# Performance work log

Measured on AMD Instinct MI355X. Metric: run time of the kernel, lower is better.

## Reference

```python
import jax, jax.numpy as jnp
import numpy as np

N0 = 16384; F_IN = 384; H = 512; E0 = 131072
DEPTH = 2; RATIO = 0.25; START_K = 6; K_INC = 1; INTERP_K = 6


def _pdist2(a, b):
    # squared euclidean distances [Na, Nb]
    d2 = jnp.sum(a * a, axis=1)[:, None] + jnp.sum(b * b, axis=1)[None, :] - 2.0 * (a @ b.T)
    return jnp.maximum(d2, 0.0)


def _fps(pos, n_keep):
    # farthest point sampling, deterministic start at node 0
    sel0 = jnp.zeros((n_keep,), jnp.int32)
    dist0 = jnp.sum((pos - pos[0]) ** 2, axis=-1)

    def body(i, st):
        sel, dist = st
        idx = jnp.argmax(dist).astype(jnp.int32)
        sel = sel.at[i].set(idx)
        dist = jnp.minimum(dist, jnp.sum((pos - pos[idx]) ** 2, axis=-1))
        return (sel, dist)

    sel, _ = jax.lax.fori_loop(1, n_keep, body, (sel0, dist0))
    return sel


def _knn_graph(pos, k):
    n = pos.shape[0]
    d2 = _pdist2(pos, pos)
    d2 = d2.at[jnp.arange(n), jnp.arange(n)].set(1e10)  # exclude self
    _, nbr = jax.lax.top_k(-d2, k)                      # [n, k] nearest neighbors
    src = nbr.reshape(-1)                               # flow: source_to_target
    dst = jnp.repeat(jnp.arange(n, dtype=nbr.dtype), k)
    return src, dst


def _gcn(x, src, dst, W, b):
    # GCNConv(improved=True): A_hat = D^-1/2 (A + 2I) D^-1/2, edge weights = 1
    n = x.shape[0]
    h = x @ W
    deg = jax.ops.segment_sum(jnp.ones(src.shape[0], x.dtype), dst, num_segments=n) + 2.0
    dinv = jax.lax.rsqrt(deg)
    coef = dinv[src] * dinv[dst]
    agg = jax.ops.segment_sum(h[src] * coef[:, None], dst, num_segments=n)
    agg = agg + h * (2.0 * dinv * dinv)[:, None]        # self loops with weight 2
    return agg + b


def _knn_interpolate(x, pos_x, pos_y, k):
    # interpolate coarse features x at pos_x onto fine positions pos_y (PyG knn_interpolate)
    d2 = _pdist2(pos_y, pos_x)                          # [Ny, Nx]
    negd, idx = jax.lax.top_k(-d2, k)                   # k nearest coarse points
    w = 1.0 / jnp.maximum(-negd, 1e-16)                 # [Ny, k]
    num = jnp.einsum('yk,ykf->yf', w, x[idx])
    return num / jnp.sum(w, axis=-1, keepdims=True)


def setup_inputs() -> dict:
    key = jax.random.key(0)
    ks = jax.random.split(key, 16)
    def w(k, fin, fout):
        return (jax.random.normal(k, (fin, fout), jnp.float32) / np.sqrt(fin)).astype(jnp.float32)
    return {
        'x': jax.random.normal(ks[0], (N0, F_IN), jnp.float32),
        'pos': jax.random.uniform(ks[1], (N0, 2), jnp.float32) * 100.0,
        'edge_index': jax.random.randint(ks[2], (2, E0), 0, N0, dtype=jnp.int32),
        'W_down0': w(ks[3], F_IN, H), 'b_down0': jnp.zeros((H,), jnp.float32),
        'W_down1': w(ks[4], H, H),   'b_down1': jnp.zeros((H,), jnp.float32),
        'W_up0': w(ks[5], H, H),     'b_up0': jnp.zeros((H,), jnp.float32),
        'W_up1': w(ks[6], H, H),     'b_up1': jnp.zeros((H,), jnp.float32),
        'W_lin': w(ks[7], H, H),     'b_lin': jnp.zeros((H,), jnp.float32),
    }


def reference(x, pos, edge_index, W_down0, b_down0, W_down1, b_down1,
              W_up0, b_up0, W_up1, b_up1, W_lin, b_lin):
    src, dst = edge_index[0], edge_index[1]
    Wd = [(W_down0, b_down0), (W_down1, b_down1)]
    Wu = [(W_up0, b_up0), (W_up1, b_up1)]
    all_pos = [pos]
    all_edges = [(src, dst)]
    for i in range(DEPTH):
        x = jax.nn.relu(_gcn(x, src, dst, *Wd[i]))
        n_keep = int(x.shape[0] * RATIO)
        perm = _fps(jax.lax.stop_gradient(pos), n_keep)
        pos = pos[perm]
        src, dst = _knn_graph(pos, START_K + i * K_INC)
        x = x[perm]
        all_pos.append(pos)
        all_edges.append((src, dst))
    for i in range(DEPTH):
        x = _knn_interpolate(x, all_pos[-i - 1], all_pos[-i - 2], INTERP_K)
        s, d = all_edges[-i - 2]
        x = jax.nn.relu(_gcn(x, s, d, *Wu[i]))
    return x @ W_lin + b_lin
```

## Files before the change

### kernel.cpp

```cpp
#include <hip/hip_runtime.h>

#define N0 16384
#define N1 4096
#define N2 1024
#define E0C 131072
#define FIN 384
#define HF 512

__device__ inline float4 f4fma(float w, const float4 v, float4 a) {
  a.x = fmaf(w, v.x, a.x); a.y = fmaf(w, v.y, a.y);
  a.z = fmaf(w, v.z, a.z); a.w = fmaf(w, v.w, a.w);
  return a;
}

__global__ __launch_bounds__(256)
void count_deg(const int* __restrict__ dst, int* __restrict__ cnt, int E) {
  int e = blockIdx.x * 256 + threadIdx.x;
  if (e < E) atomicAdd(&cnt[dst[e]], 1);
}

__global__ __launch_bounds__(1024)
void scan_offsets(const int* __restrict__ cnt, int* __restrict__ offs,
                  float* __restrict__ dinv) {
  __shared__ int ts[1024];
  const int t = threadIdx.x;
  int local[16];
  int sum = 0;
  #pragma unroll
  for (int j = 0; j < 16; ++j) { local[j] = cnt[t * 16 + j]; sum += local[j]; }
  ts[t] = sum;
  __syncthreads();
  for (int off = 1; off < 1024; off <<= 1) {
    int v = (t >= off) ? ts[t - off] : 0;
    __syncthreads();
    ts[t] += v;
    __syncthreads();
  }
  int run = ts[t] - sum;
  #pragma unroll
  for (int j = 0; j < 16; ++j) {
    offs[t * 16 + j] = run;
    dinv[t * 16 + j] = 1.0f / sqrtf((float)local[j] + 2.0f);
    run += local[j];
  }
  if (t == 1023) offs[N0] = run;
}

__global__ __launch_bounds__(256)
void fill_csr(const int* __restrict__ src, const int* __restrict__ dst,
              const int* __restrict__ offs, int* __restrict__ cursor,
              int* __restrict__ srcl, int E) {
  int e = blockIdx.x * 256 + threadIdx.x;
  if (e < E) {
    int d = dst[e];
    int p = atomicAdd(&cursor[d], 1);
    srcl[offs[d] + p] = src[e];
  }
}

template<int BM, int BN, int BK>
__global__ __launch_bounds__(256)
void gemm_f32(const float* __restrict__ A, const float* __restrict__ W,
              const float* __restrict__ bias, float* __restrict__ C,
              int M, int N, int K, int addBias) {
  __shared__ float As[BK][BM + 4];
  __shared__ float Ws[BK][BN];
  const int tid = threadIdx.x;
  const int bm = blockIdx.x * BM;
  const int bn = blockIdx.y * BN;
  const int tx = tid & 15;
  const int ty = tid >> 4;
  float acc[8][4];
  #pragma unroll
  for (int i = 0; i < 8; ++i)
    #pragma unroll
    for (int j = 0; j < 4; ++j) acc[i][j] = 0.f;

  for (int k0 = 0; k0 < K; k0 += BK) {
    #pragma unroll
    for (int h = 0; h < (BM * BK) / (256 * 4); ++h) {
      int q = tid + h * 256;
      int r = q >> 2;
      int c = (q & 3) << 2;
      float4 v = *(const float4*)(A + (size_t)(bm + r) * K + k0 + c);
      As[c][r] = v.x; As[c + 1][r] = v.y; As[c + 2][r] = v.z; As[c + 3][r] = v.w;
    }
    {
      int kk = tid >> 4;
      int n = (tid & 15) << 2;
      *(float4*)(&Ws[kk][n]) = *(const float4*)(W + (size_t)(k0 + kk) * N + bn + n);
    }
    __syncthreads();
    #pragma unroll
    for (int kk = 0; kk < BK; ++kk) {
      float4 b4 = *(const float4*)(&Ws[kk][tx << 2]);
      float4 a0 = *(const float4*)(&As[kk][ty << 3]);
      float4 a1 = *(const float4*)(&As[kk][(ty << 3) + 4]);
      float a[8] = {a0.x, a0.y, a0.z, a0.w, a1.x, a1.y, a1.z, a1.w};
      float b[4] = {b4.x, b4.y, b4.z, b4.w};
      #pragma unroll
      for (int i = 0; i < 8; ++i)
        #pragma unroll
        for (int j = 0; j < 4; ++j)
          acc[i][j] = fmaf(a[i], b[j], acc[i][j]);
    }
    __syncthreads();
  }
  #pragma unroll
  for (int i = 0; i < 8; ++i) {
    int row = bm + (ty << 3) + i;
    float4 o = {acc[i][0], acc[i][1], acc[i][2], acc[i][3]};
    if (addBias) {
      const float4 bb = *(const float4*)(bias + bn + (tx << 2));
      o.x += bb.x; o.y += bb.y; o.z += bb.z; o.w += bb.w;
    }
    *(float4*)(C + (size_t)row * N + bn + (tx << 2)) = o;
  }
}

__global__ __launch_bounds__(256)
void gcn_agg_csr(const float* __restrict__ h, const int* __restrict__ offs,
                 const int* __restrict__ srcl, const float* __restrict__ dinv,
                 const float* __restrict__ bias, float* __restrict__ out, int n) {
  const int wid = threadIdx.x >> 6, lane = threadIdx.x & 63;
  const int node = blockIdx.x * 4 + wid;
  if (node >= n) return;
  const float di = dinv[node];
  const int s0 = offs[node], s1 = offs[node + 1];
  float4 a0 = {0, 0, 0, 0}, a1 = {0, 0, 0, 0};
  for (int e = s0; e < s1; ++e) {
    const int s = srcl[e];
    const float w = dinv[s] * di;
    const float4* r = (const float4*)(h + (size_t)s * HF);
    a0 = f4fma(w, r[lane], a0);
    a1 = f4fma(w, r[64 + lane], a1);
  }
  const float sw = 2.0f * di * di;
  const float4* rs = (const float4*)(h + (size_t)node * HF);
  a0 = f4fma(sw, rs[lane], a0);
  a1 = f4fma(sw, rs[64 + lane], a1);
  const float4 b0 = *(const float4*)(bias + (lane << 2));
  const float4 b1 = *(const float4*)(bias + 256 + (lane << 2));
  a0.x = fmaxf(a0.x + b0.x, 0.f); a0.y = fmaxf(a0.y + b0.y, 0.f);
  a0.z = fmaxf(a0.z + b0.z, 0.f); a0.w = fmaxf(a0.w + b0.w, 0.f);
  a1.x = fmaxf(a1.x + b1.x, 0.f); a1.y = fmaxf(a1.y + b1.y, 0.f);
  a1.z = fmaxf(a1.z + b1.z, 0.f); a1.w = fmaxf(a1.w + b1.w, 0.f);
  float4* o = (float4*)(out + (size_t)node * HF);
  o[lane] = a0; o[64 + lane] = a1;
}

template<int K>
__global__ __launch_bounds__(256)
void gcn_agg_knn(const float* __restrict__ h, const int* __restrict__ nbr,
                 const float* __restrict__ bias, float* __restrict__ out, int n) {
  const int wid = threadIdx.x >> 6, lane = threadIdx.x & 63;
  const int node = blockIdx.x * 4 + wid;
  if (node >= n) return;
  const float di = 1.0f / sqrtf((float)(K + 2));
  const float w = di * di;
  float4 a0 = {0, 0, 0, 0}, a1 = {0, 0, 0, 0};
  #pragma unroll
  for (int j = 0; j < K; ++j) {
    const int s = nbr[node * K + j];
    const float4* r = (const float4*)(h + (size_t)s * HF);
    a0 = f4fma(w, r[lane], a0);
    a1 = f4fma(w, r[64 + lane], a1);
  }
  const float sw = 2.0f * di * di;
  const float4* rs = (const float4*)(h + (size_t)node * HF);
  a0 = f4fma(sw, rs[lane], a0);
  a1 = f4fma(sw, rs[64 + lane], a1);
  const float4 b0 = *(const float4*)(bias + (lane << 2));
  const float4 b1 = *(const float4*)(bias + 256 + (lane << 2));
  a0.x = fmaxf(a0.x + b0.x, 0.f); a0.y = fmaxf(a0.y + b0.y, 0.f);
  a0.z = fmaxf(a0.z + b0.z, 0.f); a0.w = fmaxf(a0.w + b0.w, 0.f);
  a1.x = fmaxf(a1.x + b1.x, 0.f); a1.y = fmaxf(a1.y + b1.y, 0.f);
  a1.z = fmaxf(a1.z + b1.z, 0.f); a1.w = fmaxf(a1.w + b1.w, 0.f);
  float4* o = (float4*)(out + (size_t)node * HF);
  o[lane] = a0; o[64 + lane] = a1;
}

__global__ __launch_bounds__(256)
void bin_hist(const float* __restrict__ pos, int* __restrict__ cid,
              int* __restrict__ hist, int n) {
  int i = blockIdx.x * 256 + threadIdx.x;
  if (i >= n) return;
  float x = pos[2 * i], y = pos[2 * i + 1];
  int cxi = (int)(x * 0.32f); cxi = cxi < 0 ? 0 : (cxi > 31 ? 31 : cxi);
  int cyi = (int)(y * 0.32f); cyi = cyi < 0 ? 0 : (cyi > 31 ? 31 : cyi);
  int c = cyi * 32 + cxi;
  cid[i] = c;
  atomicAdd(&hist[c], 1);
}

__global__ __launch_bounds__(1024)
void bin_scan(const int* __restrict__ hist, int* __restrict__ offs) {
  __shared__ int ts[1024];
  const int t = threadIdx.x;
  int v = hist[t];
  ts[t] = v;
  __syncthreads();
  for (int off = 1; off < 1024; off <<= 1) {
    int u = (t >= off) ? ts[t - off] : 0;
    __syncthreads();
    ts[t] += u;
    __syncthreads();
  }
  offs[t] = ts[t] - v;
  if (t == 1023) offs[1024] = ts[t];
}

__global__ __launch_bounds__(256)
void bin_scatter(const float* __restrict__ pos, const int* __restrict__ cid,
                 const int* __restrict__ offs, int* __restrict__ cursor,
                 float* __restrict__ sx, float* __restrict__ sy,
                 int* __restrict__ sid, int n) {
  int i = blockIdx.x * 256 + threadIdx.x;
  if (i >= n) return;
  int c = cid[i];
  int p = atomicAdd(&cursor[c], 1);
  int slot = offs[c] + p;
  sx[slot] = pos[2 * i];
  sy[slot] = pos[2 * i + 1];
  sid[slot] = i;
}

template<int NN>
__device__ __forceinline__ unsigned ror16(unsigned v) {
  return (unsigned)__builtin_amdgcn_update_dpp(0, (int)v, 0x120 | NN, 0xF, 0xF, false);
}

template<int N, int NCH, int NKEEP>
__global__ __launch_bounds__(NCH)
void fps_fast(const float* __restrict__ pos0,
              const float* __restrict__ sx, const float* __restrict__ sy,
              const int* __restrict__ sid,
              int* __restrict__ perm, float* __restrict__ pos_out) {
  constexpr int CHUNK = N / NCH;
  const int t = threadIdx.x;
  const int base = t * CHUNK;

  __shared__ float pxl[N];
  __shared__ float pyl[N];
  __shared__ unsigned long long ck[NCH];
  __shared__ float2 cp[NCH];
  __shared__ float bc[2];

  float d[CHUNK];
  unsigned kid[CHUNK];
  float xmn = 3.4e38f, xmx = -3.4e38f, ymn = 3.4e38f, ymx = -3.4e38f;

  float cx = pos0[0], cy = pos0[1];
  if (t == 0) { perm[0] = 0; pos_out[0] = cx; pos_out[1] = cy; }

  {
    unsigned long long best = 0; float bx = 0.f, by = 0.f;
    #pragma unroll
    for (int j = 0; j < CHUNK; ++j) {
      float qx = sx[base + j], qy = sy[base + j];
      kid[j] = ~(unsigned)sid[base + j];
      pxl[j * NCH + t] = qx;
      pyl[j * NCH + t] = qy;
      xmn = fminf(xmn, qx); xmx = fmaxf(xmx, qx);
      ymn = fminf(ymn, qy); ymx = fmaxf(ymx, qy);
      float dx = __fsub_rn(qx, cx), dy = __fsub_rn(qy, cy);
      float nd = __fadd_rn(__fmul_rn(dx, dx), __fmul_rn(dy, dy));
      d[j] = nd;
      unsigned long long kv =
          ((unsigned long long)__float_as_uint(nd) << 32) | kid[j];
      if (kv > best) { best = kv; bx = qx; by = qy; }
    }
    ck[t] = best;
    cp[t] = make_float2(bx, by);
  }
  float cmax = __uint_as_float((unsigned)(ck[t] >> 32));
  __syncthreads();

  for (int i = 1; i < NKEEP; ++i) {
    if (t < 64) {
      unsigned long long bk = 0;
      int sl = 0;
      #pragma unroll
      for (int j = 0; j < NCH / 64; ++j) {
        unsigned long long k = ck[t + j * 64];
        if (k > bk) { bk = k; sl = t + j * 64; }
      }
      {
        unsigned hi, lo, ohi, olo; int os;
        hi = (unsigned)(bk >> 32); lo = (unsigned)bk;
        ohi = ror16<1>(hi); olo = ror16<1>(lo); os = (int)ror16<1>((unsigned)sl);
        { unsigned long long ok = ((unsigned long long)ohi << 32) | olo;
          if (ok > bk) { bk = ok; sl = os; } }
        hi = (unsigned)(bk >> 32); lo = (unsigned)bk;
        ohi = ror16<2>(hi); olo = ror16<2>(lo); os = (int)ror16<2>((unsigned)sl);
        { unsigned long long ok = ((unsigned long long)ohi << 32) | olo;
          if (ok > bk) { bk = ok; sl = os; } }
        hi = (unsigned)(bk >> 32); lo = (unsigned)bk;
        ohi = ror16<4>(hi); olo = ror16<4>(lo); os = (int)ror16<4>((unsigned)sl);
        { unsigned long long ok = ((unsigned long long)ohi << 32) | olo;
          if (ok > bk) { bk = ok; sl = os; } }
        hi = (unsigned)(bk >> 32); lo = (unsigned)bk;
        ohi = ror16<8>(hi); olo = ror16<8>(lo); os = (int)ror16<8>((unsigned)sl);
        { unsigned long long ok = ((unsigned long long)ohi << 32) | olo;
          if (ok > bk) { bk = ok; sl = os; } }
      }
      unsigned hi = (unsigned)(bk >> 32), lo = (unsigned)bk;
      unsigned long long fb = 0; int fs = 0;
      #pragma unroll
      for (int r = 0; r < 4; ++r) {
        unsigned h = (unsigned)__builtin_amdgcn_readlane((int)hi, r * 16);
        unsigned l = (unsigned)__builtin_amdgcn_readlane((int)lo, r * 16);
        int s = __builtin_amdgcn_readlane(sl, r * 16);
        unsigned long long k = ((unsigned long long)h << 32) | l;
        if (k > fb) { fb = k; fs = s; }
      }
      if (t == 0) {
        float2 c = cp[fs];
        perm[i] = (int)(~(unsigned)fb);
        pos_out[2 * i] = c.x; pos_out[2 * i + 1] = c.y;
        bc[0] = c.x; bc[1] = c.y;
      }
    }
    __syncthreads();
    cx = bc[0]; cy = bc[1];

    float mdx = fmaxf(fmaxf(__fsub_rn(xmn, cx), __fsub_rn(cx, xmx)), 0.f);
    float mdy = fmaxf(fmaxf(__fsub_rn(ymn, cy), __fsub_rn(cy, ymx)), 0.f);
    float mb = mdx * mdx + mdy * mdy;
    if (!(mb * 0.99999f > cmax)) {
      unsigned long long best = 0; float bx = 0.f, by = 0.f;
      #pragma unroll
      for (int j = 0; j < CHUNK; ++j) {
        float qx = pxl[j * NCH + t], qy = pyl[j * NCH + t];
        float dx = __fsub_rn(qx, cx), dy = __fsub_rn(qy, cy);
        float nd = __fadd_rn(__fmul_rn(dx, dx), __fmul_rn(dy, dy));
        float dn = fminf(d[j], nd);
        d[j] = dn;
        unsigned long long kv =
            ((unsigned long long)__float_as_uint(dn) << 32) | kid[j];
        if (kv > best) { best = kv; bx = qx; by = qy; }
      }
      ck[t] = best;
      cp[t] = make_float2(bx, by);
      cmax = __uint_as_float((unsigned)(best >> 32));
    }
    __syncthreads();
  }
}

__global__ __launch_bounds__(256)
void gather_rows(const float* __restrict__ xin, const int* __restrict__ perm,
                 float* __restrict__ xout, int n) {
  const int wid = threadIdx.x >> 6, lane = threadIdx.x & 63;
  const int i = blockIdx.x * 4 + wid;
  if (i >= n) return;
  const int s = perm[i];
  const float4* r = (const float4*)(xin + (size_t)s * HF);
  float4* o = (float4*)(xout + (size_t)i * HF);
  o[lane] = r[lane];
  o[64 + lane] = r[64 + lane];
}

template<int NPTS, int K>
__global__ __launch_bounds__(256)
void knn_graph_kernel(const float* __restrict__ pos, int* __restrict__ srcout) {
  __shared__ float sx[NPTS], sy[NPTS], ss[NPTS];
  const int tid = threadIdx.x;
  for (int idx = tid; idx < NPTS; idx += 256) {
    float x = pos[2 * idx], y = pos[2 * idx + 1];
    sx[idx] = x; sy[idx] = y;
    ss[idx] = __fadd_rn(__fmul_rn(x, x), __fmul_rn(y, y));
  }
  __syncthreads();
  const int q = blockIdx.x * 256 + tid;
  const float qx = sx[q], qy = sy[q], qs = ss[q];
  float bd[K]; int bi[K];
  #pragma unroll
  for (int m = 0; m < K; ++m) { bd[m] = 3.4e38f; bi[m] = 0; }
  for (int j = 0; j < NPTS; ++j) {
    if (j == q) continue;
    float dot = __fadd_rn(__fmul_rn(qx, sx[j]), __fmul_rn(qy, sy[j]));
    float d2 = fmaxf(__fsub_rn(__fadd_rn(qs, ss[j]), __fmul_rn(2.0f, dot)), 0.0f);
    if (d2 < bd[K - 1]) {
      bool pr[K];
      #pragma unroll
      for (int m = 0; m < K; ++m) pr[m] = (d2 < bd[m]);
      #pragma unroll
      for (int m = K - 1; m >= 1; --m) {
        bd[m] = pr[m] ? (pr[m - 1] ? bd[m - 1] : d2) : bd[m];
        bi[m] = pr[m] ? (pr[m - 1] ? bi[m - 1] : j) : bi[m];
      }
      if (pr[0]) { bd[0] = d2; bi[0] = j; }
    }
  }
  #pragma unroll
  for (int m = 0; m < K; ++m) srcout[q * K + m] = bi[m];
}

template<int NX, int K>
__global__ __launch_bounds__(256)
void interp_topk(const float* __restrict__ posy, const float* __restrict__ posx,
                 int* __restrict__ oidx, float* __restrict__ ow,
                 float* __restrict__ owsum) {
  __shared__ float sx[NX], sy[NX], ss[NX];
  const int tid = threadIdx.x;
  for (int idx = tid; idx < NX; idx += 256) {
    float x = posx[2 * idx], y = posx[2 * idx + 1];
    sx[idx] = x; sy[idx] = y;
    ss[idx] = __fadd_rn(__fmul_rn(x, x), __fmul_rn(y, y));
  }
  __syncthreads();
  const int q = blockIdx.x * 256 + tid;
  const float qx = posy[2 * q], qy = posy[2 * q + 1];
  const float qs = __fadd_rn(__fmul_rn(qx, qx), __fmul_rn(qy, qy));
  float bd[K]; int bi[K];
  #pragma unroll
  for (int m = 0; m < K; ++m) { bd[m] = 3.4e38f; bi[m] = 0; }
  for (int j = 0; j < NX; ++j) {
    float dot = __fadd_rn(__fmul_rn(qx, sx[j]), __fmul_rn(qy, sy[j]));
    float d2 = fmaxf(__fsub_rn(__fadd_rn(qs, ss[j]), __fmul_rn(2.0f, dot)), 0.0f);
    if (d2 < bd[K - 1]) {
      bool pr[K];
      #pragma unroll
      for (int m = 0; m < K; ++m) pr[m] = (d2 < bd[m]);
      #pragma unroll
      for (int m = K - 1; m >= 1; --m) {
        bd[m] = pr[m] ? (pr[m - 1] ? bd[m - 1] : d2) : bd[m];
        bi[m] = pr[m] ? (pr[m - 1] ? bi[m - 1] : j) : bi[m];
      }
      if (pr[0]) { bd[0] = d2; bi[0] = j; }
    }
  }
  float wsum = 0.f;
  #pragma unroll
  for (int m = 0; m < K; ++m) {
    float w = 1.0f / fmaxf(bd[m], 1e-16f);
    ow[q * K + m] = w;
    oidx[q * K + m] = bi[m];
    wsum = __fadd_rn(wsum, w);
  }
  owsum[q] = wsum;
}

template<int K>
__global__ __launch_bounds__(256)
void interp_combine(const float* __restrict__ xin, const int* __restrict__ idx,
                    const float* __restrict__ w, const float* __restrict__ wsum,
                    float* __restrict__ out, int ny) {
  const int wid = threadIdx.x >> 6, lane = threadIdx.x & 63;
  const int q = blockIdx.x * 4 + wid;
  if (q >= ny) return;
  float4 a0 = {0, 0, 0, 0}, a1 = {0, 0, 0, 0};
  #pragma unroll
  for (int m = 0; m < K; ++m) {
    const int s = idx[q * K + m];
    const float wk = w[q * K + m];
    const float4* r = (const float4*)(xin + (size_t)s * HF);
    a0 = f4fma(wk, r[lane], a0);
    a1 = f4fma(wk, r[64 + lane], a1);
  }
  const float inv = wsum[q];
  a0.x /= inv; a0.y /= inv; a0.z /= inv; a0.w /= inv;
  a1.x /= inv; a1.y /= inv; a1.z /= inv; a1.w /= inv;
  float4* o = (float4*)(out + (size_t)q * HF);
  o[lane] = a0; o[64 + lane] = a1;
}

extern "C" void kernel_launch(void* const* d_in, const int* in_sizes, int n_in,
                              void* d_out, int out_size, void* d_ws, size_t ws_size,
                              hipStream_t stream) {
  const float* x    = (const float*)d_in[0];
  const float* pos  = (const float*)d_in[1];
  const int*   ei   = (const int*)d_in[2];
  const float* Wd0  = (const float*)d_in[3];
  const float* bd0  = (const float*)d_in[4];
  const float* Wd1  = (const float*)d_in[5];
  const float* bd1  = (const float*)d_in[6];
  const float* Wu0  = (const float*)d_in[7];
  const float* bu0  = (const float*)d_in[8];
  const float* Wu1  = (const float*)d_in[9];
  const float* bu1  = (const float*)d_in[10];
  const float* Wl   = (const float*)d_in[11];
  const float* bl   = (const float*)d_in[12];
  float* out = (float*)d_out;

  char* ws = (char*)d_ws;
  size_t off = 0;
  auto alloc = [&](size_t bytes) -> char* {
    char* p = ws + off;
    off = (off + bytes + 255) & ~(size_t)255;
    return p;
  };
  float* bufA   = (float*)alloc((size_t)N0 * HF * 4);
  float* bufB   = (float*)alloc((size_t)N0 * HF * 4);
  float* bufC   = (float*)alloc((size_t)N1 * HF * 4);
  float* x2     = (float*)alloc((size_t)N2 * HF * 4);
  int*   offs0  = (int*)alloc((N0 + 1) * 4);
  int*   srcl0  = (int*)alloc(E0C * 4);
  int*   cnt    = (int*)alloc(N0 * 4);
  int*   cursor = (int*)alloc(N0 * 4);
  float* dinv0  = (float*)alloc(N0 * 4);
  int*   perm0  = (int*)alloc(N1 * 4);
  float* pos1   = (float*)alloc(N1 * 2 * 4);
  int*   src1   = (int*)alloc(N1 * 6 * 4);
  int*   perm1  = (int*)alloc(N2 * 4);
  float* pos2   = (float*)alloc(N2 * 2 * 4);
  int*   iidx   = (int*)alloc((size_t)N0 * 6 * 4);
  float* iw     = (float*)alloc((size_t)N0 * 6 * 4);
  float* iwsum  = (float*)alloc(N0 * 4);
  float* bsx    = (float*)alloc(N0 * 4);
  float* bsy    = (float*)alloc(N0 * 4);
  int*   bsid   = (int*)alloc(N0 * 4);
  int*   bcid   = (int*)alloc(N0 * 4);
  int*   bhist  = (int*)alloc(1024 * 4);
  int*   bcur   = (int*)alloc(1024 * 4);
  int*   boffs  = (int*)alloc(1025 * 4);

  float* h1   = bufB;
  float* x1f  = bufB + (size_t)N1 * HF;
  float* hu0  = bufB;
  float* xu0f = bufB + (size_t)N1 * HF;

  hipMemsetAsync(cnt, 0, N0 * 4, stream);
  hipMemsetAsync(cursor, 0, N0 * 4, stream);
  count_deg<<<E0C / 256, 256, 0, stream>>>(ei + E0C, cnt, E0C);
  scan_offsets<<<1, 1024, 0, stream>>>(cnt, offs0, dinv0);
  fill_csr<<<E0C / 256, 256, 0, stream>>>(ei, ei + E0C, offs0, cursor, srcl0, E0C);

  hipMemsetAsync(bhist, 0, 1024 * 4, stream);
  hipMemsetAsync(bcur, 0, 1024 * 4, stream);
  bin_hist<<<N0 / 256, 256, 0, stream>>>(pos, bcid, bhist, N0);
  bin_scan<<<1, 1024, 0, stream>>>(bhist, boffs);
  bin_scatter<<<N0 / 256, 256, 0, stream>>>(pos, bcid, boffs, bcur, bsx, bsy, bsid, N0);

  gemm_f32<128, 64, 16><<<dim3(N0 / 128, HF / 64), 256, 0, stream>>>(
      x, Wd0, nullptr, bufA, N0, HF, FIN, 0);
  gcn_agg_csr<<<N0 / 4, 256, 0, stream>>>(bufA, offs0, srcl0, dinv0, bd0, bufB, N0);
  fps_fast<N0, 1024, N1><<<1, 1024, 0, stream>>>(pos, bsx, bsy, bsid, perm0, pos1);
  gather_rows<<<N1 / 4, 256, 0, stream>>>(bufB, perm0, bufC, N1);
  knn_graph_kernel<N1, 6><<<N1 / 256, 256, 0, stream>>>(pos1, src1);

  hipMemsetAsync(bhist, 0, 1024 * 4, stream);
  hipMemsetAsync(bcur, 0, 1024 * 4, stream);
  bin_hist<<<N1 / 256, 256, 0, stream>>>(pos1, bcid, bhist, N1);
  bin_scan<<<1, 1024, 0, stream>>>(bhist, boffs);
  bin_scatter<<<N1 / 256, 256, 0, stream>>>(pos1, bcid, boffs, bcur, bsx, bsy, bsid, N1);

  gemm_f32<128, 64, 16><<<dim3(N1 / 128, HF / 64), 256, 0, stream>>>(
      bufC, Wd1, nullptr, h1, N1, HF, HF, 0);
  gcn_agg_knn<6><<<N1 / 4, 256, 0, stream>>>(h1, src1, bd1, x1f, N1);
  fps_fast<N1, 256, N2><<<1, 256, 0, stream>>>(pos1, bsx, bsy, bsid, perm1, pos2);
  gather_rows<<<N2 / 4, 256, 0, stream>>>(x1f, perm1, x2, N2);

  interp_topk<N2, 6><<<N1 / 256, 256, 0, stream>>>(pos1, pos2, iidx, iw, iwsum);
  interp_combine<6><<<N1 / 4, 256, 0, stream>>>(x2, iidx, iw, iwsum, bufC, N1);
  gemm_f32<128, 64, 16><<<dim3(N1 / 128, HF / 64), 256, 0, stream>>>(
      bufC, Wu0, nullptr, hu0, N1, HF, HF, 0);
  gcn_agg_knn<6><<<N1 / 4, 256, 0, stream>>>(hu0, src1, bu0, xu0f, N1);

  interp_topk<N1, 6><<<N0 / 256, 256, 0, stream>>>(pos, pos1, iidx, iw, iwsum);
  interp_combine<6><<<N0 / 4, 256, 0, stream>>>(xu0f, iidx, iw, iwsum, bufA, N0);
  gemm_f32<128, 64, 16><<<dim3(N0 / 128, HF / 64), 256, 0, stream>>>(
      bufA, Wu1, nullptr, bufB, N0, HF, HF, 0);
  gcn_agg_csr<<<N0 / 4, 256, 0, stream>>>(bufB, offs0, srcl0, dinv0, bu1, bufA, N0);

  gemm_f32<128, 64, 16><<<dim3(N0 / 128, HF / 64), 256, 0, stream>>>(
      bufA, Wl, bl, out, N0, HF, HF, 1);
}
```

Measured before the change: 8.045 ms.

## Rework FPS reduction to one barrier per iteration with distributed argmax

The farthest-point-sampling kernel now reduces the per-thread best key and coordinates with DPP inside each wave (plus a small cross-wave step when there are 16 waves). It writes per-wave winners to a double-buffered shared array so every thread redoes the final 16-way reduction itself, which removes the second __syncthreads and the serial lane-0 step per iteration. Per-point distance and index are packed into one 64-bit key, and whole waves skip work via ballot when no lane's bounding box can change. The cost is redundant reduction work in every thread, and the 1024-thread variant adds an extra shared-memory exchange inside each wave.

After: 9.260 ms. +15.1%, slower.

```diff
diff --git a/kernel.cpp b/kernel.cpp
--- a/kernel.cpp
+++ b/kernel.cpp
@@ -230,121 +230,122 @@
   return (unsigned)__builtin_amdgcn_update_dpp(0, (int)v, 0x120 | NN, 0xF, 0xF, false);
 }
 
-template<int N, int NCH, int NKEEP>
-__global__ __launch_bounds__(NCH)
-void fps_fast(const float* __restrict__ pos0,
-              const float* __restrict__ sx, const float* __restrict__ sy,
-              const int* __restrict__ sid,
-              int* __restrict__ perm, float* __restrict__ pos_out) {
-  constexpr int CHUNK = N / NCH;
+__device__ __forceinline__ void kcmp(unsigned& hi, unsigned& lo, float& x, float& y,
+                                     unsigned ohi, unsigned olo, float ox, float oy) {
+  unsigned long long a = ((unsigned long long)hi << 32) | lo;
+  unsigned long long b = ((unsigned long long)ohi << 32) | olo;
+  if (b > a) { hi = ohi; lo = olo; x = ox; y = oy; }
+}
+
+#define ROR_STEP(NN) { \
+    unsigned ohi_ = ror16<NN>(hi), olo_ = ror16<NN>(lo); \
+    unsigned ox_ = ror16<NN>(__float_as_uint(x)), oy_ = ror16<NN>(__float_as_uint(y)); \
+    kcmp(hi, lo, x, y, ohi_, olo_, __uint_as_float(ox_), __uint_as_float(oy_)); }
+
+template<bool WENT>
+__device__ __forceinline__ void entry_reduce(unsigned long long ckey, float ccx, float ccy,
+                                             int t, float4* wsc,
+                                             unsigned& ehi, unsigned& elo,
+                                             float& ex, float& ey) {
+  unsigned hi = (unsigned)(ckey >> 32), lo = (unsigned)ckey;
+  float x = ccx, y = ccy;
+  ROR_STEP(1) ROR_STEP(2) ROR_STEP(4) ROR_STEP(8)
+  if constexpr (WENT) {
+    if ((t & 15) == 0)
+      wsc[(t >> 4) & 3] = make_float4(__uint_as_float(hi), __uint_as_float(lo), x, y);
+    float4 a0 = wsc[0], a1 = wsc[1], a2 = wsc[2], a3 = wsc[3];
+    hi = __float_as_uint(a0.x); lo = __float_as_uint(a0.y); x = a0.z; y = a0.w;
+    kcmp(hi, lo, x, y, __float_as_uint(a1.x), __float_as_uint(a1.y), a1.z, a1.w);
+    kcmp(hi, lo, x, y, __float_as_uint(a2.x), __float_as_uint(a2.y), a2.z, a2.w);
+    kcmp(hi, lo, x, y, __float_as_uint(a3.x), __float_as_uint(a3.y), a3.z, a3.w);
+  }
+  ehi = hi; elo = lo; ex = x; ey = y;
+}
+
+template<int N, int NT, int NKEEP>
+__global__ __launch_bounds__(NT)
+void fps_fast2(const float* __restrict__ pos0,
+               const float* __restrict__ sx, const float* __restrict__ sy,
+               const int* __restrict__ sid,
+               int* __restrict__ perm, float* __restrict__ pos_out) {
+  constexpr int CHUNK = N / NT;
+  constexpr int NWAVE = NT / 64;
+  constexpr bool WENT = (NWAVE == 16);
   const int t = threadIdx.x;
   const int base = t * CHUNK;
 
   __shared__ float pxl[N];
   __shared__ float pyl[N];
-  __shared__ unsigned long long ck[NCH];
-  __shared__ float2 cp[NCH];
-  __shared__ float bc[2];
-
-  float d[CHUNK];
-  unsigned kid[CHUNK];
-  float xmn = 3.4e38f, xmx = -3.4e38f, ymn = 3.4e38f, ymx = -3.4e38f;
-
+  __shared__ float4 ebuf[2][16];
+  __shared__ float4 wscr[NWAVE][4];
+
+  unsigned long long key[CHUNK];
   float cx = pos0[0], cy = pos0[1];
   if (t == 0) { perm[0] = 0; pos_out[0] = cx; pos_out[1] = cy; }
 
-  {
-    unsigned long long best = 0; float bx = 0.f, by = 0.f;
-    #pragma unroll
-    for (int j = 0; j < CHUNK; ++j) {
-      float qx = sx[base + j], qy = sy[base + j];
-      kid[j] = ~(unsigned)sid[base + j];
-      pxl[j * NCH + t] = qx;
-      pyl[j * NCH + t] = qy;
-      xmn = fminf(xmn, qx); xmx = fmaxf(xmx, qx);
-      ymn = fminf(ymn, qy); ymx = fmaxf(ymx, qy);
-      float dx = __fsub_rn(qx, cx), dy = __fsub_rn(qy, cy);
-      float nd = __fadd_rn(__fmul_rn(dx, dx), __fmul_rn(dy, dy));
-      d[j] = nd;
-      unsigned long long kv =
-          ((unsigned long long)__float_as_uint(nd) << 32) | kid[j];
-      if (kv > best) { best = kv; bx = qx; by = qy; }
-    }
-    ck[t] = best;
-    cp[t] = make_float2(bx, by);
-  }
-  float cmax = __uint_as_float((unsigned)(ck[t] >> 32));
+  float bx0 = 3.4e38f, bx1 = -3.4e38f, by0 = 3.4e38f, by1 = -3.4e38f;
+  unsigned long long ckey = 0; float ccx = 0.f, ccy = 0.f;
+  #pragma unroll
+  for (int j = 0; j < CHUNK; ++j) {
+    float qx = sx[base + j], qy = sy[base + j];
+    unsigned uid = ~(unsigned)sid[base + j];
+    pxl[j * NT + t] = qx; pyl[j * NT + t] = qy;
+    bx0 = fminf(bx0, qx); bx1 = fmaxf(bx1, qx);
+    by0 = fminf(by0, qy); by1 = fmaxf(by1, qy);
+    float dx = __fsub_rn(qx, cx), dy = __fsub_rn(qy, cy);
+    float nd = __fadd_rn(__fmul_rn(dx, dx), __fmul_rn(dy, dy));
+    unsigned long long k = ((unsigned long long)__float_as_uint(nd) << 32) | uid;
+    key[j] = k;
+    if (k > ckey) { ckey = k; ccx = qx; ccy = qy; }
+  }
+  float cmax = __uint_as_float((unsigned)(ckey >> 32));
+
+  unsigned ehi, elo; float ex, ey;
+  entry_reduce<WENT>(ckey, ccx, ccy, t, wscr[t >> 6], ehi, elo, ex, ey);
+  if ((t & (WENT ? 63 : 15)) == 0)
+    ebuf[0][WENT ? (t >> 6) : (t >> 4)] =
+        make_float4(__uint_as_float(ehi), __uint_as_float(elo), ex, ey);
   __syncthreads();
 
+  int p = 0;
   for (int i = 1; i < NKEEP; ++i) {
-    if (t < 64) {
-      unsigned long long bk = 0;
-      int sl = 0;
-      #pragma unroll
-      for (int j = 0; j < NCH / 64; ++j) {
-        unsigned long long k = ck[t + j * 64];
-        if (k > bk) { bk = k; sl = t + j * 64; }
+    float4 e = ebuf[p][t & 15];
+    unsigned hi = __float_as_uint(e.x), lo = __float_as_uint(e.y);
+    float x = e.z, y = e.w;
+    ROR_STEP(1) ROR_STEP(2) ROR_STEP(4) ROR_STEP(8)
+    if (t == 0) {
+      perm[i] = (int)(~lo);
+      pos_out[2 * i] = x; pos_out[2 * i + 1] = y;
+    }
+    cx = x; cy = y;
+
+    float mdx = fmaxf(fmaxf(__fsub_rn(bx0, cx), __fsub_rn(cx, bx1)), 0.f);
+    float mdy = fmaxf(fmaxf(__fsub_rn(by0, cy), __fsub_rn(cy, by1)), 0.f);
+    float mb = mdx * mdx + mdy * mdy;
+    bool act = !(mb * 0.99999f > cmax);
+    if (__ballot(act) != 0) {
+      if (act) {
+        unsigned long long best = 0; float bx = 0.f, by = 0.f;
+        #pragma unroll
+        for (int j = 0; j < CHUNK; ++j) {
+          float qx = pxl[j * NT + t], qy = pyl[j * NT + t];
+          float dx = __fsub_rn(qx, cx), dy = __fsub_rn(qy, cy);
+          float nd = __fadd_rn(__fmul_rn(dx, dx), __fmul_rn(dy, dy));
+          unsigned long long nk =
+              ((unsigned long long)__float_as_uint(nd) << 32) | (unsigned)key[j];
+          if (nk < key[j]) key[j] = nk;
+          if (key[j] > best) { best = key[j]; bx = qx; by = qy; }
+        }
+        ckey = best; ccx = bx; ccy = by;
+        cmax = __uint_as_float((unsigned)(best >> 32));
       }
-      {
-        unsigned hi, lo, ohi, olo; int os;
-        hi = (unsigned)(bk >> 32); lo = (unsigned)bk;
-        ohi = ror16<1>(hi); olo = ror16<1>(lo); os = (int)ror16<1>((unsigned)sl);
-        { unsigned long long ok = ((unsigned long long)ohi << 32) | olo;
-          if (ok > bk) { bk = ok; sl = os; } }
-        hi = (unsigned)(bk >> 32); lo = (unsigned)bk;
-        ohi = ror16<2>(hi); olo = ror16<2>(lo); os = (int)ror16<2>((unsigned)sl);
-        { unsigned long long ok = ((unsigned long long)ohi << 32) | olo;
-          if (ok > bk) { bk = ok; sl = os; } }
-        hi = (unsigned)(bk >> 32); lo = (unsigned)bk;
-        ohi = ror16<4>(hi); olo = ror16<4>(lo); os = (int)ror16<4>((unsigned)sl);
-        { unsigned long long ok = ((unsigned long long)ohi << 32) | olo;
-          if (ok > bk) { bk = ok; sl = os; } }
-        hi = (unsigned)(bk >> 32); lo = (unsigned)bk;
-        ohi = ror16<8>(hi); olo = ror16<8>(lo); os = (int)ror16<8>((unsigned)sl);
-        { unsigned long long ok = ((unsigned long long)ohi << 32) | olo;
-          if (ok > bk) { bk = ok; sl = os; } }
-      }
-      unsigned hi = (unsigned)(bk >> 32), lo = (unsigned)bk;
-      unsigned long long fb = 0; int fs = 0;
-      #pragma unroll
-      for (int r = 0; r < 4; ++r) {
-        unsigned h = (unsigned)__builtin_amdgcn_readlane((int)hi, r * 16);
-        unsigned l = (unsigned)__builtin_amdgcn_readlane((int)lo, r * 16);
-        int s = __builtin_amdgcn_readlane(sl, r * 16);
-        unsigned long long k = ((unsigned long long)h << 32) | l;
-        if (k > fb) { fb = k; fs = s; }
-      }
-      if (t == 0) {
-        float2 c = cp[fs];
-        perm[i] = (int)(~(unsigned)fb);
-        pos_out[2 * i] = c.x; pos_out[2 * i + 1] = c.y;
-        bc[0] = c.x; bc[1] = c.y;
-      }
-    }
-    __syncthreads();
-    cx = bc[0]; cy = bc[1];
-
-    float mdx = fmaxf(fmaxf(__fsub_rn(xmn, cx), __fsub_rn(cx, xmx)), 0.f);
-    float mdy = fmaxf(fmaxf(__fsub_rn(ymn, cy), __fsub_rn(cy, ymx)), 0.f);
-    float mb = mdx * mdx + mdy * mdy;
-    if (!(mb * 0.99999f > cmax)) {
-      unsigned long long best = 0; float bx = 0.f, by = 0.f;
-      #pragma unroll
-      for (int j = 0; j < CHUNK; ++j) {
-        float qx = pxl[j * NCH + t], qy = pyl[j * NCH + t];
-        float dx = __fsub_rn(qx, cx), dy = __fsub_rn(qy, cy);
-        float nd = __fadd_rn(__fmul_rn(dx, dx), __fmul_rn(dy, dy));
-        float dn = fminf(d[j], nd);
-        d[j] = dn;
-        unsigned long long kv =
-            ((unsigned long long)__float_as_uint(dn) << 32) | kid[j];
-        if (kv > best) { best = kv; bx = qx; by = qy; }
-      }
-      ck[t] = best;
-      cp[t] = make_float2(bx, by);
-      cmax = __uint_as_float((unsigned)(best >> 32));
-    }
-    __syncthreads();
+      entry_reduce<WENT>(ckey, ccx, ccy, t, wscr[t >> 6], ehi, elo, ex, ey);
+    }
+    if ((t & (WENT ? 63 : 15)) == 0)
+      ebuf[p ^ 1][WENT ? (t >> 6) : (t >> 4)] =
+          make_float4(__uint_as_float(ehi), __uint_as_float(elo), ex, ey);
+    __syncthreads();
+    p ^= 1;
   }
 }
 
@@ -536,7 +537,7 @@
   gemm_f32<128, 64, 16><<<dim3(N0 / 128, HF / 64), 256, 0, stream>>>(
       x, Wd0, nullptr, bufA, N0, HF, FIN, 0);
   gcn_agg_csr<<<N0 / 4, 256, 0, stream>>>(bufA, offs0, srcl0, dinv0, bd0, bufB, N0);
-  fps_fast<N0, 1024, N1><<<1, 1024, 0, stream>>>(pos, bsx, bsy, bsid, perm0, pos1);
+  fps_fast2<N0, 1024, N1><<<1, 1024, 0, stream>>>(pos, bsx, bsy, bsid, perm0, pos1);
   gather_rows<<<N1 / 4, 256, 0, stream>>>(bufB, perm0, bufC, N1);
   knn_graph_kernel<N1, 6><<<N1 / 256, 256, 0, stream>>>(pos1, src1);
 
@@ -549,7 +550,7 @@
   gemm_f32<128, 64, 16><<<dim3(N1 / 128, HF / 64), 256, 0, stream>>>(
       bufC, Wd1, nullptr, h1, N1, HF, HF, 0);
   gcn_agg_knn<6><<<N1 / 4, 256, 0, stream>>>(h1, src1, bd1, x1f, N1);
-  fps_fast<N1, 256, N2><<<1, 256, 0, stream>>>(pos1, bsx, bsy, bsid, perm1, pos2);
+  fps_fast2<N1, 256, N2><<<1, 256, 0, stream>>>(pos1, bsx, bsy, bsid, perm1, pos2);
   gather_rows<<<N2 / 4, 256, 0, stream>>>(x1f, perm1, x2, N2);
 
   interp_topk<N2, 6><<<N1 / 256, 256, 0, stream>>>(pos1, pos2, iidx, iw, iwsum);
```

## Morton-order spatial bins and pack FPS distances into 64-bit keys with fewer threads

Applied to the files above, without the earlier changes.

Spatial bins are now numbered in Z-order (Morton) instead of row-major, so each thread's contiguous chunk of sorted points is spatially tighter and its bounding-box skip test fires more often. The FPS kernel stores the running min distance and id together as one 64-bit key per point, which drops the separate distance and id arrays and compares keys directly. The level-0 FPS now uses 512 threads with 32 points each instead of 1024 with 16, with launch bounds set for one block. The aim is cheaper per-iteration reductions and syncs in this serial kernel, at the cost of more per-thread work and register pressure.

After: 10.61 ms. +31.9%, slower.

```diff
diff --git a/kernel.cpp b/kernel.cpp
--- a/kernel.cpp
+++ b/kernel.cpp
@@ -180,6 +180,15 @@
   o[lane] = a0; o[64 + lane] = a1;
 }
 
+__device__ __forceinline__ unsigned part1by1(unsigned x) {
+  x &= 0xFFFFu;
+  x = (x | (x << 8)) & 0x00FF00FFu;
+  x = (x | (x << 4)) & 0x0F0F0F0Fu;
+  x = (x | (x << 2)) & 0x33333333u;
+  x = (x | (x << 1)) & 0x55555555u;
+  return x;
+}
+
 __global__ __launch_bounds__(256)
 void bin_hist(const float* __restrict__ pos, int* __restrict__ cid,
               int* __restrict__ hist, int n) {
@@ -188,7 +197,7 @@
   float x = pos[2 * i], y = pos[2 * i + 1];
   int cxi = (int)(x * 0.32f); cxi = cxi < 0 ? 0 : (cxi > 31 ? 31 : cxi);
   int cyi = (int)(y * 0.32f); cyi = cyi < 0 ? 0 : (cyi > 31 ? 31 : cyi);
-  int c = cyi * 32 + cxi;
+  int c = (int)(part1by1((unsigned)cxi) | (part1by1((unsigned)cyi) << 1));
   cid[i] = c;
   atomicAdd(&hist[c], 1);
 }
@@ -230,45 +239,42 @@
   return (unsigned)__builtin_amdgcn_update_dpp(0, (int)v, 0x120 | NN, 0xF, 0xF, false);
 }
 
-template<int N, int NCH, int NKEEP>
-__global__ __launch_bounds__(NCH)
-void fps_fast(const float* __restrict__ pos0,
-              const float* __restrict__ sx, const float* __restrict__ sy,
-              const int* __restrict__ sid,
-              int* __restrict__ perm, float* __restrict__ pos_out) {
-  constexpr int CHUNK = N / NCH;
+template<int N, int NT, int NKEEP>
+__global__ __launch_bounds__(NT, 1)
+void fps_fast10(const float* __restrict__ pos0,
+                const float* __restrict__ sx, const float* __restrict__ sy,
+                const int* __restrict__ sid,
+                int* __restrict__ perm, float* __restrict__ pos_out) {
+  constexpr int CHUNK = N / NT;
   const int t = threadIdx.x;
   const int base = t * CHUNK;
 
   __shared__ float pxl[N];
   __shared__ float pyl[N];
-  __shared__ unsigned long long ck[NCH];
-  __shared__ float2 cp[NCH];
+  __shared__ unsigned long long ck[NT];
+  __shared__ float2 cp[NT];
   __shared__ float bc[2];
 
-  float d[CHUNK];
-  unsigned kid[CHUNK];
-  float xmn = 3.4e38f, xmx = -3.4e38f, ymn = 3.4e38f, ymx = -3.4e38f;
+  unsigned long long key[CHUNK];
 
   float cx = pos0[0], cy = pos0[1];
   if (t == 0) { perm[0] = 0; pos_out[0] = cx; pos_out[1] = cy; }
 
+  float x0 = 3.4e38f, x1 = -3.4e38f, y0 = 3.4e38f, y1 = -3.4e38f;
   {
     unsigned long long best = 0; float bx = 0.f, by = 0.f;
     #pragma unroll
     for (int j = 0; j < CHUNK; ++j) {
       float qx = sx[base + j], qy = sy[base + j];
-      kid[j] = ~(unsigned)sid[base + j];
-      pxl[j * NCH + t] = qx;
-      pyl[j * NCH + t] = qy;
-      xmn = fminf(xmn, qx); xmx = fmaxf(xmx, qx);
-      ymn = fminf(ymn, qy); ymx = fmaxf(ymx, qy);
+      unsigned uid = ~(unsigned)sid[base + j];
+      pxl[j * NT + t] = qx; pyl[j * NT + t] = qy;
+      x0 = fminf(x0, qx); x1 = fmaxf(x1, qx);
+      y0 = fminf(y0, qy); y1 = fmaxf(y1, qy);
       float dx = __fsub_rn(qx, cx), dy = __fsub_rn(qy, cy);
       float nd = __fadd_rn(__fmul_rn(dx, dx), __fmul_rn(dy, dy));
-      d[j] = nd;
-      unsigned long long kv =
-          ((unsigned long long)__float_as_uint(nd) << 32) | kid[j];
-      if (kv > best) { best = kv; bx = qx; by = qy; }
+      unsigned long long k = ((unsigned long long)__float_as_uint(nd) << 32) | uid;
+      key[j] = k;
+      if (k > best) { best = k; bx = qx; by = qy; }
     }
     ck[t] = best;
     cp[t] = make_float2(bx, by);
@@ -281,7 +287,7 @@
       unsigned long long bk = 0;
       int sl = 0;
       #pragma unroll
-      for (int j = 0; j < NCH / 64; ++j) {
+      for (int j = 0; j < NT / 64; ++j) {
         unsigned long long k = ck[t + j * 64];
         if (k > bk) { bk = k; sl = t + j * 64; }
       }
@@ -324,21 +330,20 @@
     __syncthreads();
     cx = bc[0]; cy = bc[1];
 
-    float mdx = fmaxf(fmaxf(__fsub_rn(xmn, cx), __fsub_rn(cx, xmx)), 0.f);
-    float mdy = fmaxf(fmaxf(__fsub_rn(ymn, cy), __fsub_rn(cy, ymx)), 0.f);
+    float mdx = fmaxf(fmaxf(__fsub_rn(x0, cx), __fsub_rn(cx, x1)), 0.f);
+    float mdy = fmaxf(fmaxf(__fsub_rn(y0, cy), __fsub_rn(cy, y1)), 0.f);
     float mb = mdx * mdx + mdy * mdy;
     if (!(mb * 0.99999f > cmax)) {
       unsigned long long best = 0; float bx = 0.f, by = 0.f;
       #pragma unroll
       for (int j = 0; j < CHUNK; ++j) {
-        float qx = pxl[j * NCH + t], qy = pyl[j * NCH + t];
+        float qx = pxl[j * NT + t], qy = pyl[j * NT + t];
         float dx = __fsub_rn(qx, cx), dy = __fsub_rn(qy, cy);
         float nd = __fadd_rn(__fmul_rn(dx, dx), __fmul_rn(dy, dy));
-        float dn = fminf(d[j], nd);
-        d[j] = dn;
-        unsigned long long kv =
-            ((unsigned long long)__float_as_uint(dn) << 32) | kid[j];
-        if (kv > best) { best = kv; bx = qx; by = qy; }
+        unsigned long long nk =
+            ((unsigned long long)__float_as_uint(nd) << 32) | (unsigned)key[j];
+        if (nk < key[j]) key[j] = nk;
+        if (key[j] > best) { best = key[j]; bx = qx; by = qy; }
       }
       ck[t] = best;
       cp[t] = make_float2(bx, by);
@@ -536,7 +541,7 @@
   gemm_f32<128, 64, 16><<<dim3(N0 / 128, HF / 64), 256, 0, stream>>>(
       x, Wd0, nullptr, bufA, N0, HF, FIN, 0);
   gcn_agg_csr<<<N0 / 4, 256, 0, stream>>>(bufA, offs0, srcl0, dinv0, bd0, bufB, N0);
-  fps_fast<N0, 1024, N1><<<1, 1024, 0, stream>>>(pos, bsx, bsy, bsid, perm0, pos1);
+  fps_fast10<N0, 512, N1><<<1, 512, 0, stream>>>(pos, bsx, bsy, bsid, perm0, pos1);
   gather_rows<<<N1 / 4, 256, 0, stream>>>(bufB, perm0, bufC, N1);
   knn_graph_kernel<N1, 6><<<N1 / 256, 256, 0, stream>>>(pos1, src1);
 
@@ -549,7 +554,7 @@
   gemm_f32<128, 64, 16><<<dim3(N1 / 128, HF / 64), 256, 0, stream>>>(
       bufC, Wd1, nullptr, h1, N1, HF, HF, 0);
   gcn_agg_knn<6><<<N1 / 4, 256, 0, stream>>>(h1, src1, bd1, x1f, N1);
-  fps_fast<N1, 256, N2><<<1, 256, 0, stream>>>(pos1, bsx, bsy, bsid, perm1, pos2);
+  fps_fast10<N1, 256, N2><<<1, 256, 0, stream>>>(pos1, bsx, bsy, bsid, perm1, pos2);
   gather_rows<<<N2 / 4, 256, 0, stream>>>(x1f, perm1, x2, N2);
 
   interp_topk<N2, 6><<<N1 / 256, 256, 0, stream>>>(pos1, pos2, iidx, iw, iwsum);
```
